# Kernel tuning notes

Measured on AMD Instinct MI355X. Metric: run time of the kernel, lower is better.

## Reference

```python
import jax, jax.numpy as jnp
import numpy as np

TIME_STEP = 0.1  # matches module-level time_step in the torch source
STEPS = 65536


def setup_inputs() -> dict:
    key = jax.random.key(0)
    k1, k2 = jax.random.split(key)
    x = jax.random.normal(k1, (12,), dtype=jnp.float32)          # initial state [pos(6), vel(6)]
    actions = jax.random.normal(k2, (STEPS, 6), dtype=jnp.float32)  # learned per-step accelerations
    return {"x": x, "actions": actions}


def reference(x, actions):
    dt = jnp.float32(TIME_STEP)
    half_dt2 = jnp.float32(0.5) * dt * dt

    def step(state, a):
        # state: [12] = [pos(6), vel(6)]; a: [6]
        pos = state[:6] + state[6:] * dt + half_dt2 * a
        vel = state[6:] + dt * a
        new_state = jnp.concatenate([pos, vel])
        return new_state, new_state

    _, states = jax.lax.scan(step, x, actions)  # states: [steps, 12]
    return (states, actions)
```

## Files before the change

### kernel.cpp

```cpp
#include <hip/hip_runtime.h>


#define STEPS   65536
#define NCH     6
#define STATE   12
#define NB      256
#define CHUNK   (STEPS / NB)
#define BLK     (NCH * 64)
#define ACT_OFF (STEPS * STATE)

__global__ __launch_bounds__(BLK) void k_partial(const float4* __restrict__ act4,
                                                 float4* __restrict__ outact4,
                                                 double* __restrict__ bsum) {
    __shared__ float sIn[CHUNK * NCH];
    const int b = blockIdx.x, tid = threadIdx.x;

    float4 v = act4[b * (CHUNK * NCH / 4) + tid];
    outact4[b * (CHUNK * NCH / 4) + tid] = v;
    ((float4*)sIn)[tid] = v;
    __syncthreads();

    const int c = tid >> 6, lane = tid & 63;
    double sA = 0.0, sW = 0.0;
#pragma unroll
    for (int k = 0; k < 4; ++k) {
        const int   tl = k * 64 + lane;
        const float a  = sIn[tl * NCH + c];
        sA += (double)a;
        sW += (double)(b * CHUNK + tl) * (double)a;
    }
#pragma unroll
    for (int off = 32; off > 0; off >>= 1) {
        sA += __shfl_down(sA, off, 64);
        sW += __shfl_down(sW, off, 64);
    }
    if (lane == 0) {
        bsum[(b * NCH + c) * 2 + 0] = sA;
        bsum[(b * NCH + c) * 2 + 1] = sW;
    }
}

__global__ __launch_bounds__(BLK) void k_final(const float4* __restrict__ act4,
                                               const float* __restrict__ x,
                                               const double* __restrict__ bsum,
                                               float4* __restrict__ out4) {
    __shared__ float sIn[CHUNK * NCH];
    __shared__ float sOut[CHUNK * STATE];
    const int b = blockIdx.x, tid = threadIdx.x;

    ((float4*)sIn)[tid] = act4[b * (CHUNK * NCH / 4) + tid];
    __syncthreads();

    const int c = tid >> 6, lane = tid & 63;

    double offA, offW;
    {
        double vA = 0.0, vW = 0.0;
#pragma unroll
        for (int k = 0; k < 4; ++k) {
            const int idx = k * 64 + lane;
            if (idx < b) {
                vA += bsum[(idx * NCH + c) * 2 + 0];
                vW += bsum[(idx * NCH + c) * 2 + 1];
            }
        }
#pragma unroll
        for (int off = 32; off > 0; off >>= 1) {
            vA += __shfl_down(vA, off, 64);
            vW += __shfl_down(vW, off, 64);
        }
        offA = __shfl(vA, 0, 64);
        offW = __shfl(vW, 0, 64);
    }

    const double dt  = (double)0.1f;
    const double dt2 = dt * dt;
    const double p0  = (double)x[c];
    const double v0  = (double)x[NCH + c];

    double accA = offA, accW = offW;
#pragma unroll
    for (int k = 0; k < 4; ++k) {
        const int   tl = k * 64 + lane;
        const int   t  = b * CHUNK + tl;
        const float a  = sIn[tl * NCH + c];
        double iA = (double)a;
        double iW = (double)t * (double)a;
#pragma unroll
        for (int off = 1; off < 64; off <<= 1) {
            const double uA = __shfl_up(iA, off, 64);
            const double uW = __shfl_up(iW, off, 64);
            if (lane >= off) { iA += uA; iW += uW; }
        }
        const double runA = accA + iA;
        const double runW = accW + iW;
        const double vel = v0 + dt * runA;
        const double pos = p0 + dt * (double)(t + 1) * v0
                         + dt2 * (((double)t + 0.5) * runA - runW);
        sOut[tl * STATE + c]       = (float)pos;
        sOut[tl * STATE + NCH + c] = (float)vel;
        accA += __shfl(iA, 63, 64);
        accW += __shfl(iW, 63, 64);
    }
    __syncthreads();

    const float4* so4 = (const float4*)sOut;
    out4[b * (CHUNK * STATE / 4) + tid]       = so4[tid];
    out4[b * (CHUNK * STATE / 4) + BLK + tid] = so4[BLK + tid];
}

extern "C" void kernel_launch(void* const* d_in, const int* in_sizes, int n_in,
                              void* d_out, int out_size, void* d_ws, size_t ws_size,
                              hipStream_t stream) {
    const float* x       = (const float*)d_in[0];
    const float* actions = (const float*)d_in[1];
    float*       out     = (float*)d_out;
    double*      bsum    = (double*)d_ws;

    hipLaunchKernelGGL(k_partial, dim3(NB), dim3(BLK), 0, stream,
                       (const float4*)actions, (float4*)(out + ACT_OFF), bsum);
    hipLaunchKernelGGL(k_final, dim3(NB), dim3(BLK), 0, stream,
                       (const float4*)actions, x, bsum, (float4*)out);
}
```

Before: 62.37 us.

## Fuse partial-sum and final scan kernels via cooperative grid sync

Merges the two-pass block-sum and scan kernels into one cooperative kernel that uses a grid-wide barrier between the block-partial phase and the prefix phase. Block partials go to a device global array instead of the workspace. This removes one kernel launch and the second reload of actions into shared memory. In exchange it pays for a cooperative launch and a grid-wide sync, which can be costly on a GPU with many XCDs.

```diff
diff --git a/kernel.cpp b/kernel.cpp
--- a/kernel.cpp
+++ b/kernel.cpp
@@ -1,4 +1,7 @@
 #include <hip/hip_runtime.h>
+#include <hip/hip_cooperative_groups.h>
+
+namespace cg = cooperative_groups;
 
 
 #define STEPS   65536
@@ -9,49 +12,43 @@
 #define BLK     (NCH * 64)
 #define ACT_OFF (STEPS * STATE)
 
-__global__ __launch_bounds__(BLK) void k_partial(const float4* __restrict__ act4,
-                                                 float4* __restrict__ outact4,
-                                                 double* __restrict__ bsum) {
+__device__ double g_bsum[NB * NCH * 2];
+
+__global__ __launch_bounds__(BLK) void k_fused(const float4* __restrict__ act4,
+                                               const float* __restrict__ x,
+                                               float* __restrict__ out) {
     __shared__ float sIn[CHUNK * NCH];
+    __shared__ float sOut[CHUNK * STATE];
     const int b = blockIdx.x, tid = threadIdx.x;
 
     float4 v = act4[b * (CHUNK * NCH / 4) + tid];
-    outact4[b * (CHUNK * NCH / 4) + tid] = v;
+    ((float4*)(out + ACT_OFF))[b * (CHUNK * NCH / 4) + tid] = v;
     ((float4*)sIn)[tid] = v;
     __syncthreads();
 
     const int c = tid >> 6, lane = tid & 63;
-    double sA = 0.0, sW = 0.0;
+
+    {
+        double sA = 0.0, sW = 0.0;
 #pragma unroll
-    for (int k = 0; k < 4; ++k) {
-        const int   tl = k * 64 + lane;
-        const float a  = sIn[tl * NCH + c];
-        sA += (double)a;
-        sW += (double)(b * CHUNK + tl) * (double)a;
+        for (int k = 0; k < 4; ++k) {
+            const int   tl = k * 64 + lane;
+            const float a  = sIn[tl * NCH + c];
+            sA += (double)a;
+            sW += (double)(b * CHUNK + tl) * (double)a;
+        }
+#pragma unroll
+        for (int off = 32; off > 0; off >>= 1) {
+            sA += __shfl_down(sA, off, 64);
+            sW += __shfl_down(sW, off, 64);
+        }
+        if (lane == 0) {
+            g_bsum[(b * NCH + c) * 2 + 0] = sA;
+            g_bsum[(b * NCH + c) * 2 + 1] = sW;
+        }
     }
-#pragma unroll
-    for (int off = 32; off > 0; off >>= 1) {
-        sA += __shfl_down(sA, off, 64);
-        sW += __shfl_down(sW, off, 64);
-    }
-    if (lane == 0) {
-        bsum[(b * NCH + c) * 2 + 0] = sA;
-        bsum[(b * NCH + c) * 2 + 1] = sW;
-    }
-}
 
-__global__ __launch_bounds__(BLK) void k_final(const float4* __restrict__ act4,
-                                               const float* __restrict__ x,
-                                               const double* __restrict__ bsum,
-                                               float4* __restrict__ out4) {
-    __shared__ float sIn[CHUNK * NCH];
-    __shared__ float sOut[CHUNK * STATE];
-    const int b = blockIdx.x, tid = threadIdx.x;
-
-    ((float4*)sIn)[tid] = act4[b * (CHUNK * NCH / 4) + tid];
-    __syncthreads();
-
-    const int c = tid >> 6, lane = tid & 63;
+    cg::this_grid().sync();
 
     double offA, offW;
     {
@@ -60,8 +57,8 @@
         for (int k = 0; k < 4; ++k) {
             const int idx = k * 64 + lane;
             if (idx < b) {
-                vA += bsum[(idx * NCH + c) * 2 + 0];
-                vW += bsum[(idx * NCH + c) * 2 + 1];
+                vA += g_bsum[(idx * NCH + c) * 2 + 0];
+                vW += g_bsum[(idx * NCH + c) * 2 + 1];
             }
         }
 #pragma unroll
@@ -105,20 +102,19 @@
     __syncthreads();
 
     const float4* so4 = (const float4*)sOut;
-    out4[b * (CHUNK * STATE / 4) + tid]       = so4[tid];
-    out4[b * (CHUNK * STATE / 4) + BLK + tid] = so4[BLK + tid];
+    float4*       o4  = (float4*)out;
+    o4[b * (CHUNK * STATE / 4) + tid]       = so4[tid];
+    o4[b * (CHUNK * STATE / 4) + BLK + tid] = so4[BLK + tid];
 }
 
 extern "C" void kernel_launch(void* const* d_in, const int* in_sizes, int n_in,
                               void* d_out, int out_size, void* d_ws, size_t ws_size,
                               hipStream_t stream) {
-    const float* x       = (const float*)d_in[0];
-    const float* actions = (const float*)d_in[1];
-    float*       out     = (float*)d_out;
-    double*      bsum    = (double*)d_ws;
+    const float*  x    = (const float*)d_in[0];
+    const float4* act4 = (const float4*)d_in[1];
+    float*        out  = (float*)d_out;
 
-    hipLaunchKernelGGL(k_partial, dim3(NB), dim3(BLK), 0, stream,
-                       (const float4*)actions, (float4*)(out + ACT_OFF), bsum);
-    hipLaunchKernelGGL(k_final, dim3(NB), dim3(BLK), 0, stream,
-                       (const float4*)actions, x, bsum, (float4*)out);
+    void* args[] = { (void*)&act4, (void*)&x, (void*)&out };
+    hipLaunchCooperativeKernel((void*)k_fused, dim3(NB), dim3(BLK),
+                               args, 0, stream);
 }
```

Result: slower. 100.9 us (+61.7%).
